# Performance work log

Measured on AMD Instinct MI355X. Metric: run time of the kernel, lower is better.

Reference implementation:

```python
import jax, jax.numpy as jnp
import numpy as np

B, A, C = 16, 3, 80
INPUT_DIM = 640
GRIDS = (80, 40, 20)
NT = 256

# classic YOLOv3 anchors in pixels; divided by stride -> grid units (what the module expects)
ANCHORS_PX = np.array([[[10, 13], [16, 30], [33, 23]],
                       [[30, 61], [62, 45], [59, 119]],
                       [[116, 90], [156, 198], [373, 326]]], dtype=np.float32)


def setup_inputs() -> dict:
    key = jax.random.key(0)
    k = jax.random.split(key, 8)
    strides = np.array([INPUT_DIM / g for g in GRIDS], dtype=np.float32)  # 8,16,32
    anchors = jnp.asarray(ANCHORS_PX / strides[:, None, None])  # [3,3,2] grid units
    preds = {}
    for i, g in enumerate(GRIDS):
        preds[f"pred{i}"] = jax.random.normal(k[i], (B, A, g, g, 5 + C), dtype=jnp.float32)
    b = jax.random.randint(k[3], (NT, 1), 0, B).astype(jnp.float32)
    cls = jax.random.randint(k[4], (NT, 1), 0, C).astype(jnp.float32)
    xy = jax.random.uniform(k[5], (NT, 2), dtype=jnp.float32)
    wh = jax.random.uniform(k[6], (NT, 2), dtype=jnp.float32, minval=0.02, maxval=0.3)
    targets = jnp.concatenate([b, cls, xy, wh], axis=1)  # [NT,6] = (b, cls, x, y, w, h)
    return {**preds, "anchors": anchors, "targets": targets}


def _clog(p):
    # torch BCELoss clamps log terms at -100
    return jnp.clip(jnp.log(p), -100.0)


def _scale_loss(pred, anchors_g, targets):
    gh, gw = pred.shape[2], pred.shape[3]
    stride = INPUT_DIM / gh
    sa = anchors_g * stride  # [A,2] scaled anchors in pixels

    bi = targets[:, 0].astype(jnp.int32)
    ci = targets[:, 1].astype(jnp.int32)
    x = targets[:, 2] * gw
    y = targets[:, 3] * gh
    w = targets[:, 4] * INPUT_DIM
    h = targets[:, 5] * INPUT_DIM

    valid = (x >= 0) & (y >= 0) & (x <= gw - 1) & (y <= gh - 1)
    gx = jnp.floor(x).astype(jnp.int32)
    gy = jnp.floor(y).astype(jnp.int32)

    # vectorized IoU of (0,0,w,h) vs (0,0,aw,ah) -> best anchor per target
    inter = jnp.minimum(w[:, None], sa[None, :, 0]) * jnp.minimum(h[:, None], sa[None, :, 1])
    iou = inter / (w[:, None] * h[:, None] + sa[None, :, 0] * sa[None, :, 1] - inter + 1e-16)
    best = jnp.argmax(iou, axis=1)  # [NT]

    txv = x - gx.astype(x.dtype)
    tyv = y - gy.astype(y.dtype)
    twv = jnp.log(w / sa[best, 0] + 1e-16)
    thv = jnp.log(h / sa[best, 1] + 1e-16)

    # invalid targets -> out-of-bounds batch index, dropped by scatter
    bdrop = jnp.where(valid, bi, B)
    idx = (bdrop, best, gy, gx)
    shp = (B, A, gh, gw)
    obj = jnp.zeros(shp, dtype=bool).at[idx].set(True, mode='drop')
    tx = jnp.zeros(shp, pred.dtype).at[idx].set(txv, mode='drop')
    ty = jnp.zeros(shp, pred.dtype).at[idx].set(tyv, mode='drop')
    tw = jnp.zeros(shp, pred.dtype).at[idx].set(twv, mode='drop')
    th = jnp.zeros(shp, pred.dtype).at[idx].set(thv, mode='drop')
    tcls = jnp.zeros(shp + (C,), pred.dtype).at[idx].set(jax.nn.one_hot(ci, C, dtype=pred.dtype), mode='drop')

    m = obj.astype(pred.dtype)
    pxy = jax.nn.sigmoid(pred[..., 0:2])
    pobj = jax.nn.sigmoid(pred[..., 4])
    pcls = jax.nn.sigmoid(pred[..., 5:])

    loss_x = jnp.sum(m * (pxy[..., 0] - tx) ** 2)
    loss_y = jnp.sum(m * (pxy[..., 1] - ty) ** 2)
    loss_w = jnp.sum(m * (pred[..., 2] - tw) ** 2)
    loss_h = jnp.sum(m * (pred[..., 3] - th) ** 2)
    loss_obj = -jnp.sum(m * _clog(pobj))
    loss_noobj = -jnp.sum((1.0 - m) * _clog(1.0 - pobj))
    loss_cls = -jnp.sum(m[..., None] * (tcls * _clog(pcls) + (1.0 - tcls) * _clog(1.0 - pcls)))
    return loss_x + loss_y + loss_w + loss_h + loss_obj + 0.5 * loss_noobj + 1.0 * loss_cls


def reference(pred0, pred1, pred2, anchors, targets):
    return (_scale_loss(pred0, anchors[0], targets)
            + _scale_loss(pred1, anchors[1], targets)
            + _scale_loss(pred2, anchors[2], targets))
```

## Files before the change

### kernel.cpp

```cpp
#include <hip/hip_runtime.h>

#define BB 16
#define AA 3
#define CC 80
#define NT 256

__device__ __forceinline__ float sigf(float x){ return 1.f/(1.f+expf(-x)); }
__device__ __forceinline__ float clogf_(float p){ return fmaxf(logf(p), -100.f); }

__device__ __forceinline__ void block_reduce_atomic(float v, float* out, float scale){
    #pragma unroll
    for (int o = 32; o > 0; o >>= 1) v += __shfl_down(v, o, 64);
    __shared__ float wsum[4];
    int lane = threadIdx.x & 63;
    int wid  = threadIdx.x >> 6;
    if (lane == 0) wsum[wid] = v;
    __syncthreads();
    if (threadIdx.x == 0) {
        float s = wsum[0] + wsum[1] + wsum[2] + wsum[3];
        atomicAdd(out, s * scale);
    }
}

__global__ void zero_kernel(float* out){ out[0] = 0.f; }

__global__ void noobj_kernel(const float* __restrict__ p0, const float* __restrict__ p1,
                             const float* __restrict__ p2, float* __restrict__ out){
    const int n0 = BB*AA*80*80;
    const int n1 = BB*AA*40*40;
    int i = blockIdx.x * 256 + threadIdx.x;
    const float* p; int cell;
    if (i < n0)            { p = p0; cell = i; }
    else if (i < n0 + n1)  { p = p1; cell = i - n0; }
    else                   { p = p2; cell = i - n0 - n1; }
    float x = p[(long)cell * 85 + 4];
    float term = clogf_(1.f - sigf(x));
    block_reduce_atomic(term, out, -0.5f);
}

__global__ void targets_kernel(const float* __restrict__ p0, const float* __restrict__ p1,
                               const float* __restrict__ p2, const float* __restrict__ anchors,
                               const float* __restrict__ targets, float* __restrict__ out){
    int s = blockIdx.x;
    int g = (s == 0) ? 80 : ((s == 1) ? 40 : 20);
    const float* pred = (s == 0) ? p0 : ((s == 1) ? p1 : p2);
    float stride = 640.f / (float)g;
    int t = threadIdx.x;

    float x = targets[t*6 + 2] * (float)g;
    float y = targets[t*6 + 3] * (float)g;
    float w = targets[t*6 + 4] * 640.f;
    float h = targets[t*6 + 5] * 640.f;
    int bi = (int)targets[t*6 + 0];
    int ci = (int)targets[t*6 + 1];

    bool valid = (x >= 0.f) && (y >= 0.f) && (x <= (float)(g-1)) && (y <= (float)(g-1));
    int gx = (int)floorf(x), gy = (int)floorf(y);

    float best_iou = -1.f, saw = 1.f, sah = 1.f; int best = 0;
    #pragma unroll
    for (int a = 0; a < 3; a++){
        float aw = anchors[s*6 + a*2 + 0] * stride;
        float ah = anchors[s*6 + a*2 + 1] * stride;
        float inter = fminf(w, aw) * fminf(h, ah);
        float iou = inter / (w*h + aw*ah - inter + 1e-16f);
        if (iou > best_iou){ best_iou = iou; best = a; saw = aw; sah = ah; }
    }

    __shared__ int skey[NT];
    int key = valid ? (((bi*AA + best)*g + gy)*g + gx) : -1;
    skey[t] = key;
    __syncthreads();
    bool owner = valid;
    if (valid){
        for (int t2 = t + 1; t2 < NT; t2++){
            if (skey[t2] == key){ owner = false; break; }
        }
    }

    float acc = 0.f;
    if (owner){
        const float* pc = pred + (long)key * 85;
        float txv = x - (float)gx;
        float tyv = y - (float)gy;
        float twv = logf(w/saw + 1e-16f);
        float thv = logf(h/sah + 1e-16f);
        float px = sigf(pc[0]); acc += (px - txv)*(px - txv);
        float py = sigf(pc[1]); acc += (py - tyv)*(py - tyv);
        float dw = pc[2] - twv; acc += dw*dw;
        float dh = pc[3] - thv; acc += dh*dh;
        float pobj = sigf(pc[4]);
        acc += -clogf_(pobj);
        acc += 0.5f*clogf_(1.f - pobj);
        for (int c = 0; c < CC; c++){
            float pcv = sigf(pc[5 + c]);
            acc += -((c == ci) ? clogf_(pcv) : clogf_(1.f - pcv));
        }
    }
    block_reduce_atomic(acc, out, 1.f);
}

extern "C" void kernel_launch(void* const* d_in, const int* in_sizes, int n_in,
                              void* d_out, int out_size, void* d_ws, size_t ws_size,
                              hipStream_t stream) {
    const float* p0      = (const float*)d_in[0];
    const float* p1      = (const float*)d_in[1];
    const float* p2      = (const float*)d_in[2];
    const float* anchors = (const float*)d_in[3];
    const float* targets = (const float*)d_in[4];
    float* out = (float*)d_out;

    zero_kernel<<<1, 1, 0, stream>>>(out);
    noobj_kernel<<<1575, 256, 0, stream>>>(p0, p1, p2, out);
    targets_kernel<<<3, 256, 0, stream>>>(p0, p1, p2, anchors, targets, out);
}
```

Before: 216.3 us.

## Fuse noobj and target kernels with grid-stride loop and deterministic two-pass reduction

Merges the noobj and per-target kernels into one launch. The noobj part now uses 256 grid-stride blocks instead of 1575, and the targets part runs in three extra blocks. Each block writes its partial sum to a workspace, and a small final kernel reduces those partials, which replaces the zero kernel and the global atomics. log(1-sigmoid(x)) is computed as -log1p(exp(x)). The target path also contains a redundant anchor-index computation that is immediately overwritten. The kernel is bound by strided reads of one float per 85-float cell, so fewer blocks may reduce memory parallelism.

```diff
diff --git a/kernel.cpp b/kernel.cpp
--- a/kernel.cpp
+++ b/kernel.cpp
@@ -5,10 +5,14 @@
 #define CC 80
 #define NT 256
 
+#define NOOBJ_BLOCKS 256
+#define TOTAL_BLOCKS (NOOBJ_BLOCKS + 3)
+#define NCELL (BB*AA*(80*80 + 40*40 + 20*20))
+
 __device__ __forceinline__ float sigf(float x){ return 1.f/(1.f+expf(-x)); }
 __device__ __forceinline__ float clogf_(float p){ return fmaxf(logf(p), -100.f); }
 
-__device__ __forceinline__ void block_reduce_atomic(float v, float* out, float scale){
+__device__ __forceinline__ float block_reduce(float v){
     #pragma unroll
     for (int o = 32; o > 0; o >>= 1) v += __shfl_down(v, o, 64);
     __shared__ float wsum[4];
@@ -16,88 +20,111 @@
     int wid  = threadIdx.x >> 6;
     if (lane == 0) wsum[wid] = v;
     __syncthreads();
-    if (threadIdx.x == 0) {
-        float s = wsum[0] + wsum[1] + wsum[2] + wsum[3];
-        atomicAdd(out, s * scale);
-    }
+    return wsum[0] + wsum[1] + wsum[2] + wsum[3];
 }
 
-__global__ void zero_kernel(float* out){ out[0] = 0.f; }
-
-__global__ void noobj_kernel(const float* __restrict__ p0, const float* __restrict__ p1,
-                             const float* __restrict__ p2, float* __restrict__ out){
+__global__ void yolo_main_kernel(const float* __restrict__ p0, const float* __restrict__ p1,
+                                 const float* __restrict__ p2, const float* __restrict__ anchors,
+                                 const float* __restrict__ targets, float* __restrict__ ws){
     const int n0 = BB*AA*80*80;
     const int n1 = BB*AA*40*40;
-    int i = blockIdx.x * 256 + threadIdx.x;
-    const float* p; int cell;
-    if (i < n0)            { p = p0; cell = i; }
-    else if (i < n0 + n1)  { p = p1; cell = i - n0; }
-    else                   { p = p2; cell = i - n0 - n1; }
-    float x = p[(long)cell * 85 + 4];
-    float term = clogf_(1.f - sigf(x));
-    block_reduce_atomic(term, out, -0.5f);
+
+    float partial = 0.f;
+
+    if (blockIdx.x < NOOBJ_BLOCKS) {
+        float acc = 0.f;
+        for (int i = blockIdx.x * 256 + threadIdx.x; i < NCELL; i += NOOBJ_BLOCKS * 256) {
+            const float* p; int cell;
+            if (i < n0)            { p = p0; cell = i; }
+            else if (i < n0 + n1)  { p = p1; cell = i - n0; }
+            else                   { p = p2; cell = i - n0 - n1; }
+            float x = p[(long)cell * 85 + 4];
+            acc += fmaxf(-log1pf(expf(x)), -100.f);
+        }
+        partial = block_reduce(acc) * -0.5f;
+    } else {
+        int s = blockIdx.x - NOOBJ_BLOCKS;
+        int g = (s == 0) ? 80 : ((s == 1) ? 40 : 20);
+        const float* pred = (s == 0) ? p0 : ((s == 1) ? p1 : p2);
+        float stride = 640.f / (float)g;
+        int t = threadIdx.x;
+
+        float x = targets[t*6 + 2] * (float)g;
+        float y = targets[t*6 + 3] * (float)g;
+        float w = targets[t*6 + 4] * 640.f;
+        float h = targets[t*6 + 5] * 640.f;
+        int bi = (int)targets[t*6 + 0];
+        int ci = (int)targets[t*6 + 1];
+
+        bool valid = (x >= 0.f) && (y >= 0.f) && (x <= (float)(g-1)) && (y <= (float)(g-1));
+        int gx = (int)floorf(x), gy = (int)floorf(y);
+
+        float best_iou = -1.f, saw = 1.f, sah = 1.f;
+        #pragma unroll
+        for (int a = 0; a < 3; a++){
+            float aw = anchors[s*6 + a*2 + 0] * stride;
+            float ah = anchors[s*6 + a*2 + 1] * stride;
+            float inter = fminf(w, aw) * fminf(h, ah);
+            float iou = inter / (w*h + aw*ah - inter + 1e-16f);
+            if (iou > best_iou){ best_iou = iou; saw = aw; sah = ah; }
+        }
+
+        __shared__ int skey[NT];
+        int key = valid ? (((bi*AA + ((saw==anchors[s*6+0]*stride && sah==anchors[s*6+1]*stride) ? 0
+                                     : (saw==anchors[s*6+2]*stride && sah==anchors[s*6+3]*stride) ? 1 : 2))*g + gy)*g + gx)
+                        : -1;
+        {
+            float bi2 = -1.f; int besti = 0;
+            #pragma unroll
+            for (int a = 0; a < 3; a++){
+                float aw = anchors[s*6 + a*2 + 0] * stride;
+                float ah = anchors[s*6 + a*2 + 1] * stride;
+                float inter = fminf(w, aw) * fminf(h, ah);
+                float iou = inter / (w*h + aw*ah - inter + 1e-16f);
+                if (iou > bi2){ bi2 = iou; besti = a; }
+            }
+            key = valid ? (((bi*AA + besti)*g + gy)*g + gx) : -1;
+        }
+        skey[t] = key;
+        __syncthreads();
+        bool owner = valid;
+        if (valid){
+            for (int t2 = t + 1; t2 < NT; t2++){
+                if (skey[t2] == key){ owner = false; break; }
+            }
+        }
+
+        float acc = 0.f;
+        if (owner){
+            const float* pc = pred + (long)key * 85;
+            float txv = x - (float)gx;
+            float tyv = y - (float)gy;
+            float twv = logf(w/saw + 1e-16f);
+            float thv = logf(h/sah + 1e-16f);
+            float px = sigf(pc[0]); acc += (px - txv)*(px - txv);
+            float py = sigf(pc[1]); acc += (py - tyv)*(py - tyv);
+            float dw = pc[2] - twv; acc += dw*dw;
+            float dh = pc[3] - thv; acc += dh*dh;
+            float pobj = sigf(pc[4]);
+            acc += -clogf_(pobj);
+            acc += 0.5f*fmaxf(-log1pf(expf(pc[4])), -100.f);
+            for (int c = 0; c < CC; c++){
+                float pcv = sigf(pc[5 + c]);
+                acc += -((c == ci) ? clogf_(pcv) : clogf_(1.f - pcv));
+            }
+        }
+        partial = block_reduce(acc);
+    }
+
+    if (threadIdx.x == 0) ws[blockIdx.x] = partial;
 }
 
-__global__ void targets_kernel(const float* __restrict__ p0, const float* __restrict__ p1,
-                               const float* __restrict__ p2, const float* __restrict__ anchors,
-                               const float* __restrict__ targets, float* __restrict__ out){
-    int s = blockIdx.x;
-    int g = (s == 0) ? 80 : ((s == 1) ? 40 : 20);
-    const float* pred = (s == 0) ? p0 : ((s == 1) ? p1 : p2);
-    float stride = 640.f / (float)g;
+__global__ void yolo_final_kernel(const float* __restrict__ ws, float* __restrict__ out){
     int t = threadIdx.x;
-
-    float x = targets[t*6 + 2] * (float)g;
-    float y = targets[t*6 + 3] * (float)g;
-    float w = targets[t*6 + 4] * 640.f;
-    float h = targets[t*6 + 5] * 640.f;
-    int bi = (int)targets[t*6 + 0];
-    int ci = (int)targets[t*6 + 1];
-
-    bool valid = (x >= 0.f) && (y >= 0.f) && (x <= (float)(g-1)) && (y <= (float)(g-1));
-    int gx = (int)floorf(x), gy = (int)floorf(y);
-
-    float best_iou = -1.f, saw = 1.f, sah = 1.f; int best = 0;
-    #pragma unroll
-    for (int a = 0; a < 3; a++){
-        float aw = anchors[s*6 + a*2 + 0] * stride;
-        float ah = anchors[s*6 + a*2 + 1] * stride;
-        float inter = fminf(w, aw) * fminf(h, ah);
-        float iou = inter / (w*h + aw*ah - inter + 1e-16f);
-        if (iou > best_iou){ best_iou = iou; best = a; saw = aw; sah = ah; }
-    }
-
-    __shared__ int skey[NT];
-    int key = valid ? (((bi*AA + best)*g + gy)*g + gx) : -1;
-    skey[t] = key;
-    __syncthreads();
-    bool owner = valid;
-    if (valid){
-        for (int t2 = t + 1; t2 < NT; t2++){
-            if (skey[t2] == key){ owner = false; break; }
-        }
-    }
-
-    float acc = 0.f;
-    if (owner){
-        const float* pc = pred + (long)key * 85;
-        float txv = x - (float)gx;
-        float tyv = y - (float)gy;
-        float twv = logf(w/saw + 1e-16f);
-        float thv = logf(h/sah + 1e-16f);
-        float px = sigf(pc[0]); acc += (px - txv)*(px - txv);
-        float py = sigf(pc[1]); acc += (py - tyv)*(py - tyv);
-        float dw = pc[2] - twv; acc += dw*dw;
-        float dh = pc[3] - thv; acc += dh*dh;
-        float pobj = sigf(pc[4]);
-        acc += -clogf_(pobj);
-        acc += 0.5f*clogf_(1.f - pobj);
-        for (int c = 0; c < CC; c++){
-            float pcv = sigf(pc[5 + c]);
-            acc += -((c == ci) ? clogf_(pcv) : clogf_(1.f - pcv));
-        }
-    }
-    block_reduce_atomic(acc, out, 1.f);
+    float v = ws[t];
+    if (t < TOTAL_BLOCKS - 256) v += ws[256 + t];
+    float s = block_reduce(v);
+    if (t == 0) out[0] = s;
 }
 
 extern "C" void kernel_launch(void* const* d_in, const int* in_sizes, int n_in,
@@ -109,8 +136,8 @@
     const float* anchors = (const float*)d_in[3];
     const float* targets = (const float*)d_in[4];
     float* out = (float*)d_out;
+    float* ws  = (float*)d_ws;
 
-    zero_kernel<<<1, 1, 0, stream>>>(out);
-    noobj_kernel<<<1575, 256, 0, stream>>>(p0, p1, p2, out);
-    targets_kernel<<<3, 256, 0, stream>>>(p0, p1, p2, anchors, targets, out);
+    yolo_main_kernel<<<TOTAL_BLOCKS, 256, 0, stream>>>(p0, p1, p2, anchors, targets, ws);
+    yolo_final_kernel<<<1, 256, 0, stream>>>(ws, out);
 }
```

New measurement: 185.0 us. 14.5% less time.
